# Optimization experiments

Measured on AMD Instinct MI355X. Metric: run time of the kernel, lower is better.

Reference implementation:

```python
import jax, jax.numpy as jnp
import numpy as np

B, S, D = 2, 2048, 1024
FFN = 4096
E, TOPK = 4, 2
H, WIN = 8, 128
EPS = 1e-6


def rmsnorm(x, w):
    rms = jax.lax.rsqrt(jnp.mean(x * x, axis=-1, keepdims=True) + EPS)
    return x * rms * w


def linear_scan(x, a):
    """h_t = a_t * h_{t-1} + x_t along axis=1, via associative scan."""
    def comb(c1, c2):
        a1, x1 = c1
        a2, x2 = c2
        return (a1 * a2, a2 * x1 + x2)
    _, h = jax.lax.associative_scan(comb, (a, x), axis=1)
    return h


def mingru_expert(xn, Wg, bg, Wv, bv, Wd, bd):
    g = xn @ Wg + bg
    v = xn @ Wv + bv
    d = xn @ Wd + bd
    x_scan = jax.nn.sigmoid(g) * jnp.tanh(v)
    a = 0.001 + 0.998 * jax.nn.sigmoid(d)
    return linear_scan(x_scan, a)


def setup_inputs() -> dict:
    key = jax.random.key(0)
    ks = jax.random.split(key, 16)
    sc = 0.02
    return {
        "x": jax.random.normal(ks[0], (B, S, D), jnp.float32),
        "rms_mix_w": jnp.ones((D,), jnp.float32),
        "gate_w": jax.random.normal(ks[1], (D, E), jnp.float32) * sc,
        "Wg": jax.random.normal(ks[2], (E, D, D), jnp.float32) * sc,
        "bg": jnp.zeros((E, D), jnp.float32),
        "Wv": jax.random.normal(ks[3], (E, D, D), jnp.float32) * sc,
        "bv": jnp.zeros((E, D), jnp.float32),
        "Wd": jax.random.normal(ks[4], (E, D, D), jnp.float32) * sc,
        "bd": jnp.ones((E, D), jnp.float32),  # decay_bias_init = 1.0
        "rms_attn_w": jnp.ones((D,), jnp.float32),
        "w_qkv": jax.random.normal(ks[5], (D, 3 * D), jnp.float32) * sc,
        "w_attn_out": jax.random.normal(ks[6], (D, D), jnp.float32) * sc,
        "rms_ffn_w": jnp.ones((D,), jnp.float32),
        "w_ffn_gate": jax.random.normal(ks[7], (D, FFN), jnp.float32) * sc,
        "w_ffn_up": jax.random.normal(ks[8], (D, FFN), jnp.float32) * sc,
        "w_ffn_out": jax.random.normal(ks[9], (FFN, D), jnp.float32) * sc,
    }


def reference(x, rms_mix_w, gate_w, Wg, bg, Wv, bv, Wd, bd,
              rms_attn_w, w_qkv, w_attn_out,
              rms_ffn_w, w_ffn_gate, w_ffn_up, w_ffn_out):
    # --- MoE-MinGRU mixer -------------------------------------------------
    xn = rmsnorm(x, rms_mix_w)
    gate_logits = xn @ gate_w                         # [B,S,E]
    top_vals, top_idx = jax.lax.top_k(gate_logits, TOPK)
    weights = jax.nn.softmax(top_vals, axis=-1)       # [B,S,K]
    expert_outs = jax.vmap(mingru_expert, in_axes=(None, 0, 0, 0, 0, 0, 0))(
        xn, Wg, bg, Wv, bv, Wd, bd)                   # [E,B,S,D]
    expert_outs = jnp.moveaxis(expert_outs, 0, 2)     # [B,S,E,D]
    gathered = jnp.take_along_axis(expert_outs, top_idx[..., None], axis=2)  # [B,S,K,D]
    mix = jnp.sum(weights[..., None] * gathered, axis=2)
    x = x + mix

    # --- Sliding-window causal attention ----------------------------------
    xn = rmsnorm(x, rms_attn_w)
    dh = D // H
    qkv = (xn @ w_qkv).reshape(B, S, 3, H, dh)
    q, k, v = qkv[:, :, 0], qkv[:, :, 1], qkv[:, :, 2]  # [B,S,H,dh]
    scores = jnp.einsum("bqhd,bkhd->bhqk", q, k) / jnp.sqrt(jnp.float32(dh))
    i = jnp.arange(S)[:, None]
    j = jnp.arange(S)[None, :]
    allowed = (j <= i) & (j > i - WIN)
    scores = jnp.where(allowed, scores, -jnp.inf)
    attn = jax.nn.softmax(scores, axis=-1)
    ao = jnp.einsum("bhqk,bkhd->bqhd", attn, v).reshape(B, S, D)
    x = x + ao @ w_attn_out

    # --- SwiGLU FFN --------------------------------------------------------
    xn = rmsnorm(x, rms_ffn_w)
    ffn = (jax.nn.silu(xn @ w_ffn_gate) * (xn @ w_ffn_up)) @ w_ffn_out
    return x + ffn
```

## Files before the change

kernel.cpp:

```cpp
#include <hip/hip_runtime.h>
#include <hip/hip_bf16.h>
#include <math.h>

constexpr int kB   = 2;
constexpr int kS   = 2048;
constexpr int kD   = 1024;
constexpr int kFFN = 4096;
constexpr int kM   = kB * kS;
constexpr int kH   = 8;
constexpr int kDH  = 128;
constexpr int kNC  = 64;
constexpr int kT   = kS / kNC;
constexpr int kNE  = 12288;

typedef unsigned short u16;
typedef __attribute__((ext_vector_type(8))) short short8;
typedef __attribute__((ext_vector_type(4))) float f32x4;

__device__ __forceinline__ float sigf(float x) { return 1.0f / (1.0f + __expf(-x)); }
__device__ __forceinline__ float bu2f(u16 u) { return __uint_as_float(((unsigned)u) << 16); }
__device__ __forceinline__ u16 f2bu(float f) {
    __hip_bfloat16 h = __float2bfloat16(f);
    return reinterpret_cast<u16&>(h);
}
__device__ __forceinline__ void async16(const void* g, void* l) {
    __builtin_amdgcn_global_load_lds((const __attribute__((address_space(1))) void*)g,
                                     (__attribute__((address_space(3))) void*)l, 16, 0, 0);
}

__global__ __launch_bounds__(256) void rmsnorm_k(const float* __restrict__ x,
                                                 const float* __restrict__ w,
                                                 u16* __restrict__ o)
{
    __shared__ float red[4];
    const int row = blockIdx.x;
    const int t = threadIdx.x;
    float4 v = ((const float4*)(x + (size_t)row * kD))[t];
    float ss = v.x*v.x + v.y*v.y + v.z*v.z + v.w*v.w;
    #pragma unroll
    for (int m = 32; m; m >>= 1) ss += __shfl_xor(ss, m);
    if ((t & 63) == 0) red[t >> 6] = ss;
    __syncthreads();
    float tot = red[0] + red[1] + red[2] + red[3];
    float r = rsqrtf(tot * (1.0f / (float)kD) + 1e-6f);
    float4 wv = ((const float4*)w)[t];
    ushort4 u;
    u.x = f2bu(v.x * r * wv.x); u.y = f2bu(v.y * r * wv.y);
    u.z = f2bu(v.z * r * wv.z); u.w = f2bu(v.w * r * wv.w);
    ((ushort4*)(o + (size_t)row * kD))[t] = u;
}

__global__ __launch_bounds__(64) void routing_k(const float* __restrict__ x,
                                                const float* __restrict__ wmix,
                                                const float* __restrict__ gw,
                                                float* __restrict__ wts,
                                                int* __restrict__ idx)
{
    const int row = blockIdx.x;
    const int lane = threadIdx.x;
    const float* xr = x + (size_t)row * kD;
    float ss = 0.0f;
    for (int d = lane; d < kD; d += 64) { float v = xr[d]; ss = fmaf(v, v, ss); }
    #pragma unroll
    for (int m = 32; m; m >>= 1) ss += __shfl_xor(ss, m);
    float r = rsqrtf(ss * (1.0f / (float)kD) + 1e-6f);

    float a0 = 0, a1 = 0, a2 = 0, a3 = 0;
    for (int d = lane; d < kD; d += 64) {
        float xv = xr[d] * wmix[d];
        float4 g = ((const float4*)gw)[d];
        a0 = fmaf(xv, g.x, a0);
        a1 = fmaf(xv, g.y, a1);
        a2 = fmaf(xv, g.z, a2);
        a3 = fmaf(xv, g.w, a3);
    }
    #pragma unroll
    for (int m = 32; m; m >>= 1) {
        a0 += __shfl_xor(a0, m);
        a1 += __shfl_xor(a1, m);
        a2 += __shfl_xor(a2, m);
        a3 += __shfl_xor(a3, m);
    }
    if (lane == 0) {
        float a[4] = {a0, a1, a2, a3};
        int i0 = 0; float v0 = a[0];
        #pragma unroll
        for (int e = 1; e < 4; ++e) if (a[e] > v0) { v0 = a[e]; i0 = e; }
        int i1 = -1; float v1 = -INFINITY;
        #pragma unroll
        for (int e = 0; e < 4; ++e) if (e != i0 && a[e] > v1) { v1 = a[e]; i1 = e; }
        float e1 = __expf(r * (v1 - v0));
        float dn = 1.0f + e1;
        wts[row * 2 + 0] = 1.0f / dn;
        wts[row * 2 + 1] = e1 / dn;
        idx[row * 2 + 0] = i0;
        idx[row * 2 + 1] = i1;
    }
}

__global__ __launch_bounds__(256) void transp_k(const float* __restrict__ src,
                                                u16* __restrict__ dst,
                                                int rows, int cols,
                                                size_t sstride, size_t dstride)
{
    __shared__ float t[32][33];
    const float* s = src + blockIdx.z * sstride;
    u16* d = dst + blockIdx.z * dstride;
    const int c0 = blockIdx.x * 32, r0 = blockIdx.y * 32;
    const int tc = threadIdx.x & 31, tr4 = (threadIdx.x >> 5) * 4;
    #pragma unroll
    for (int i = 0; i < 4; ++i)
        t[tr4 + i][tc] = s[(size_t)(r0 + tr4 + i) * cols + c0 + tc];
    __syncthreads();
    #pragma unroll
    for (int i = 0; i < 4; ++i) {
        int cc = tr4 + i;
        d[(size_t)(c0 + cc) * rows + r0 + tc] = f2bu(t[tc][cc]);
    }
}

__global__ __launch_bounds__(256) void biaspack_k(const float* __restrict__ bg,
                                                  const float* __restrict__ bv,
                                                  const float* __restrict__ bd,
                                                  float* __restrict__ pb)
{
    int e = blockIdx.y;
    int r = blockIdx.x * 256 + threadIdx.x;
    const float* src = (r < 1024) ? bg : (r < 2048) ? bv : bd;
    pb[e * 3072 + r] = src[e * 1024 + (r & 1023)];
}

template<bool BIAS, bool SILU, bool MUL>
__global__ __launch_bounds__(512, 2) void gemm256_k(
    const u16* __restrict__ A, const u16* __restrict__ BT,
    const float* __restrict__ bias, const u16* __restrict__ mulsrc,
    u16* __restrict__ Cout, int N, int K)
{
    __shared__ __align__(16) u16 lds[3 * 24576];
    const int tid = threadIdx.x;
    const int l = tid & 63;
    const int w = tid >> 6;
    const int wr = w >> 1, wc = w & 1;
    const int fr = l & 15, g = l >> 4;

    const int gx = gridDim.x;
    const int nwg = gx * gridDim.y;
    const int orig = blockIdx.y * gx + blockIdx.x;
    const int xcd = orig & 7;
    const int q8 = nwg >> 3, r8 = nwg & 7;
    const int wg = (xcd < r8 ? xcd * (q8 + 1) : r8 * (q8 + 1) + (xcd - r8) * q8) + (orig >> 3);
    const int bm = (wg / gx) * 256, bn = (wg % gx) * 128;

    const int srow = l >> 3;
    const int scol = (l & 7) ^ srow;
    const u16* gA = A  + (size_t)(bm + srow) * K + scol * 8;
    const u16* gB = BT + (size_t)(bn + srow) * K + scol * 8;

    auto STAGE = [&](int kt, int sb) {
        u16* dst = lds + sb * 24576 + l * 8;
        const int k0 = kt * 64;
        #pragma unroll
        for (int i = 0; i < 4; ++i) {
            int chunk = w * 4 + i;
            async16(gA + (size_t)chunk * 8 * K + k0, dst + chunk * 512);
        }
        #pragma unroll
        for (int i = 0; i < 2; ++i) {
            int chunk = w * 2 + i;
            async16(gB + (size_t)chunk * 8 * K + k0, dst + 16384 + chunk * 512);
        }
    };

    f32x4 acc[4][4];
    #pragma unroll
    for (int m = 0; m < 4; ++m)
        #pragma unroll
        for (int n = 0; n < 4; ++n) acc[m][n] = (f32x4){0.f, 0.f, 0.f, 0.f};

    STAGE(0, 0);
    STAGE(1, 1);
    const int nt = K >> 6;
    int cs = 0;
    for (int t = 0; t < nt; ++t) {
        if (t + 1 < nt) asm volatile("s_waitcnt vmcnt(6)" ::: "memory");
        else            asm volatile("s_waitcnt vmcnt(0)" ::: "memory");
        __builtin_amdgcn_s_barrier();
        __builtin_amdgcn_sched_barrier(0);
        if (t + 2 < nt) {
            int ns = cs + 2; if (ns >= 3) ns -= 3;
            STAGE(t + 2, ns);
        }
        const u16* bA = lds + cs * 24576;
        const u16* bB = bA + 16384;
        #pragma unroll
        for (int ks = 0; ks < 2; ++ks) {
            short8 a[4], b[4];
            const int xo = ((ks * 4 + g) ^ (fr & 7)) * 8;
            #pragma unroll
            for (int m = 0; m < 4; ++m)
                a[m] = *(const short8*)(bA + (wr * 64 + m * 16 + fr) * 64 + xo);
            #pragma unroll
            for (int n = 0; n < 4; ++n)
                b[n] = *(const short8*)(bB + (wc * 64 + n * 16 + fr) * 64 + xo);
            #pragma unroll
            for (int m = 0; m < 4; ++m)
                #pragma unroll
                for (int n = 0; n < 4; ++n)
                    acc[m][n] = __builtin_amdgcn_mfma_f32_16x16x32_bf16(a[m], b[n], acc[m][n], 0, 0, 0);
        }
        cs = (cs == 2) ? 0 : cs + 1;
    }

    const int orow0 = bm + wr * 64 + g * 4;
    const int ocol0 = bn + wc * 64 + fr;
    float bi[4];
    if constexpr (BIAS) {
        #pragma unroll
        for (int n = 0; n < 4; ++n) bi[n] = bias[ocol0 + n * 16];
    }
    #pragma unroll
    for (int m = 0; m < 4; ++m) {
        #pragma unroll
        for (int r = 0; r < 4; ++r) {
            const size_t ro = (size_t)(orow0 + m * 16 + r) * N;
            #pragma unroll
            for (int n = 0; n < 4; ++n) {
                const size_t off = ro + ocol0 + n * 16;
                float v = acc[m][n][r];
                if constexpr (BIAS) v += bi[n];
                if constexpr (SILU) v = v * sigf(v);
                if constexpr (MUL)  v *= bu2f(mulsrc[off]);
                Cout[off] = f2bu(v);
            }
        }
    }
}

template<int WN, bool BIAS, bool RES, bool SILU, bool MUL, bool OBF>
__global__ __launch_bounds__(256, 2) void gemm_bf16_k(
    const u16* __restrict__ A, const u16* __restrict__ BT,
    const float* __restrict__ bias, const float* __restrict__ res,
    const u16* __restrict__ mulsrc, void* __restrict__ Cout,
    int N, int K)
{
    constexpr int BN = 32 * WN;
    __shared__ __align__(16) u16 As[2][128 * 32];
    __shared__ __align__(16) u16 Bs[2][BN * 32];
    const int tid = threadIdx.x;
    const int lane = tid & 63;
    const int w = tid >> 6;
    const int wr = w >> 1, wc = w & 1;

    const int gx = gridDim.x;
    const int nwg = gx * gridDim.y;
    const int orig = blockIdx.y * gx + blockIdx.x;
    const int xcd = orig & 7;
    const int q8 = nwg >> 3, r8 = nwg & 7;
    const int wg = (xcd < r8 ? xcd * (q8 + 1) : r8 * (q8 + 1) + (xcd - r8) * q8) + (orig >> 3);
    const int bm = (wg / gx) * 128, bn = (wg % gx) * BN;

    const int fr = lane & 15, fk = (lane >> 4) * 8;

    const u16* gA1 = A + (size_t)(bm + (tid >> 2)) * K + (tid & 3) * 8;
    const u16* gA2 = gA1 + (size_t)64 * K;
    const u16* gB1 = BT + (size_t)(bn + (tid >> 2)) * K + (tid & 3) * 8;
    const u16* gB2 = gB1 + (size_t)64 * K;

    f32x4 acc[4][WN];
    #pragma unroll
    for (int m = 0; m < 4; ++m)
        #pragma unroll
        for (int n = 0; n < WN; ++n) acc[m][n] = (f32x4){0.f, 0.f, 0.f, 0.f};

    const int paOff = (wr * 64 + fr) * 32 + fk;
    const int pbOff = (wc * WN * 16 + fr) * 32 + fk;

    async16(gA1, As[0] + tid * 8);
    async16(gA2, As[0] + (256 + tid) * 8);
    async16(gB1, Bs[0] + tid * 8);
    if constexpr (WN == 4) async16(gB2, Bs[0] + (256 + tid) * 8);
    __syncthreads();

    int cur = 0;
    for (int k0 = 0; k0 < K; k0 += 32) {
        if (k0 + 32 < K) {
            const int nb = cur ^ 1;
            async16(gA1 + k0 + 32, As[nb] + tid * 8);
            async16(gA2 + k0 + 32, As[nb] + (256 + tid) * 8);
            async16(gB1 + k0 + 32, Bs[nb] + tid * 8);
            if constexpr (WN == 4) async16(gB2 + k0 + 32, Bs[nb] + (256 + tid) * 8);
        }
        const u16* pa = As[cur] + paOff;
        const u16* pb = Bs[cur] + pbOff;
        short8 a[4], b[WN];
        #pragma unroll
        for (int m = 0; m < 4; ++m) a[m] = *(const short8*)(pa + m * 512);
        #pragma unroll
        for (int n = 0; n < WN; ++n) b[n] = *(const short8*)(pb + n * 512);
        #pragma unroll
        for (int m = 0; m < 4; ++m)
            #pragma unroll
            for (int n = 0; n < WN; ++n)
                acc[m][n] = __builtin_amdgcn_mfma_f32_16x16x32_bf16(a[m], b[n], acc[m][n], 0, 0, 0);
        __syncthreads();
        cur ^= 1;
    }

    const int orow0 = bm + wr * 64 + ((lane >> 4) << 2);
    const int ocol0 = bn + wc * WN * 16 + fr;
    float bi[WN];
    if constexpr (BIAS) {
        #pragma unroll
        for (int n = 0; n < WN; ++n) bi[n] = bias[ocol0 + n * 16];
    }
    #pragma unroll
    for (int m = 0; m < 4; ++m) {
        #pragma unroll
        for (int r = 0; r < 4; ++r) {
            const int row = orow0 + m * 16 + r;
            const size_t ro = (size_t)row * N;
            #pragma unroll
            for (int n = 0; n < WN; ++n) {
                const size_t off = ro + ocol0 + n * 16;
                float v = acc[m][n][r];
                if constexpr (BIAS) v += bi[n];
                if constexpr (SILU) v = v * sigf(v);
                if constexpr (MUL)  v *= bu2f(mulsrc[off]);
                if constexpr (RES)  v += res[off];
                if constexpr (OBF)  ((u16*)Cout)[off] = f2bu(v);
                else                ((float*)Cout)[off] = v;
            }
        }
    }
}

__global__ __launch_bounds__(256) void scan1_k(const u16* __restrict__ gvdall,
                                               float* __restrict__ sumA,
                                               float* __restrict__ sumX)
{
    const int e = blockIdx.y;
    int i = blockIdx.x * 256 + threadIdx.x;
    int d = i & (kD - 1);
    int c = (i >> 10) & (kNC - 1);
    int b = i >> 16;
    const u16* gvd = gvdall + e * 3072;
    size_t base = ((size_t)b * kS + c * kT) * kNE + d;
    float A = 1.0f, X = 0.0f;
    for (int t = 0; t < kT; ++t) {
        size_t ix = base + (size_t)t * kNE;
        float xs = sigf(bu2f(gvd[ix])) * tanhf(bu2f(gvd[ix + 1024]));
        float a  = 0.001f + 0.998f * sigf(bu2f(gvd[ix + 2048]));
        A *= a;
        X = fmaf(a, X, xs);
    }
    size_t si = ((size_t)(e * kNC + c) * kB + b) * kD + d;
    sumA[si] = A;
    sumX[si] = X;
}

__global__ __launch_bounds__(256) void scan2_k(const float* __restrict__ sumA,
                                               const float* __restrict__ sumX,
                                               float* __restrict__ carry)
{
    const int e = blockIdx.y;
    int bd = blockIdx.x * 256 + threadIdx.x;
    float h = 0.0f;
    for (int c = 0; c < kNC; ++c) {
        size_t si = ((size_t)(e * kNC + c)) * (kB * kD) + bd;
        carry[si] = h;
        h = fmaf(sumA[si], h, sumX[si]);
    }
}

__global__ __launch_bounds__(256) void scan3_k(const u16* __restrict__ gvdall,
                                               const float* __restrict__ carry,
                                               u16* __restrict__ ehb)
{
    const int e = blockIdx.y;
    int i = blockIdx.x * 256 + threadIdx.x;
    int d = i & (kD - 1);
    int c = (i >> 10) & (kNC - 1);
    int b = i >> 16;
    const u16* gvd = gvdall + e * 3072;
    size_t base = ((size_t)b * kS + c * kT) * kNE + d;
    size_t obase = (size_t)e * kM * kD + ((size_t)b * kS + c * kT) * kD + d;
    float h = carry[((size_t)(e * kNC + c) * kB + b) * kD + d];
    for (int t = 0; t < kT; ++t) {
        size_t ix = base + (size_t)t * kNE;
        float xs = sigf(bu2f(gvd[ix])) * tanhf(bu2f(gvd[ix + 1024]));
        float a  = 0.001f + 0.998f * sigf(bu2f(gvd[ix + 2048]));
        h = fmaf(a, h, xs);
        ehb[obase + (size_t)t * kD] = f2bu(h);
    }
}

__global__ __launch_bounds__(256) void mix_k(const float* __restrict__ x,
                                             const u16* __restrict__ ehb,
                                             const float* __restrict__ wts,
                                             const int* __restrict__ idx,
                                             float* __restrict__ xo)
{
    size_t i = (size_t)blockIdx.x * 256 + threadIdx.x;
    int m = (int)(i >> 8);
    float w0 = wts[m * 2 + 0], w1 = wts[m * 2 + 1];
    int e0 = idx[m * 2 + 0], e1 = idx[m * 2 + 1];
    size_t MD4 = (size_t)kM * (kD / 4);
    float4 xv = ((const float4*)x)[i];
    ushort4 h0 = ((const ushort4*)ehb)[(size_t)e0 * MD4 + i];
    ushort4 h1 = ((const ushort4*)ehb)[(size_t)e1 * MD4 + i];
    float4 o;
    o.x = xv.x + w0 * bu2f(h0.x) + w1 * bu2f(h1.x);
    o.y = xv.y + w0 * bu2f(h0.y) + w1 * bu2f(h1.y);
    o.z = xv.z + w0 * bu2f(h0.z) + w1 * bu2f(h1.z);
    o.w = xv.w + w0 * bu2f(h0.w) + w1 * bu2f(h1.w);
    ((float4*)xo)[i] = o;
}

__global__ __launch_bounds__(256) void transpV_k(const u16* __restrict__ qkvb,
                                                 u16* __restrict__ vT)
{
    __shared__ u16 t[64][68];
    const int tid = threadIdx.x;
    const int s0 = blockIdx.x * 64;
    const int d0 = blockIdx.y * 64;
    const int bh = blockIdx.z;
    const int bb = bh >> 3, hh = bh & 7;
    const u16* src = qkvb + (size_t)(bb * kS + s0) * 3072 + 2048 + hh * kDH + d0;
    for (int idx = tid; idx < 64 * 16; idx += 256) {
        int sl = idx >> 4, c4 = (idx & 15) * 4;
        *(ushort4*)&t[sl][c4] = *(const ushort4*)(src + (size_t)sl * 3072 + c4);
    }
    __syncthreads();
    u16* dst = vT + ((size_t)bh * kDH + d0) * kS + s0;
    for (int idx = tid; idx < 64 * 16; idx += 256) {
        int dl = idx >> 4, s4 = (idx & 15) * 4;
        ushort4 v;
        v.x = t[s4 + 0][dl]; v.y = t[s4 + 1][dl];
        v.z = t[s4 + 2][dl]; v.w = t[s4 + 3][dl];
        *(ushort4*)(dst + (size_t)dl * kS + s4) = v;
    }
}

__global__ __launch_bounds__(256) void attn_mfma_k(const u16* __restrict__ qkvb,
                                                   const u16* __restrict__ vT,
                                                   u16* __restrict__ aob)
{
    __shared__ __align__(16) u16 KV[26112];
    __shared__ __align__(16) u16 P[4 * 16 * 200];

    const int tid = threadIdx.x;
    const int lane = tid & 63;
    const int w = tid >> 6;
    const int fr = lane & 15, g = lane >> 4;
    const int q0 = blockIdx.x * 64;
    const int hh = blockIdx.y;
    const int bb = blockIdx.z;
    const int kbase = q0 - 128;
    const float scale = 0.08838834764831845f;

    const u16* qkv_b = qkvb + (size_t)bb * kS * 3072 + hh * kDH;

    for (int idx = tid; idx < 192 * 16; idx += 256) {
        int k = idx >> 4, c = idx & 15;
        int kg = kbase + k; if (kg < 0) kg = 0;
        short8 v = *(const short8*)(qkv_b + (size_t)kg * 3072 + 1024 + c * 8);
        *(short8*)(&KV[k * 136 + c * 8]) = v;
    }
    short8 qf[4];
    {
        const u16* qrow = qkv_b + (size_t)(q0 + w * 16 + fr) * 3072 + g * 8;
        #pragma unroll
        for (int s = 0; s < 4; ++s) qf[s] = *(const short8*)(qrow + s * 32);
    }
    __syncthreads();

    f32x4 sacc[12];
    #pragma unroll
    for (int f = 0; f < 12; ++f) sacc[f] = (f32x4){0.f, 0.f, 0.f, 0.f};
    #pragma unroll
    for (int s = 0; s < 4; ++s) {
        #pragma unroll
        for (int f = 0; f < 12; ++f) {
            short8 bfr = *(const short8*)(&KV[(f * 16 + fr) * 136 + s * 32 + g * 8]);
            sacc[f] = __builtin_amdgcn_mfma_f32_16x16x32_bf16(qf[s], bfr, sacc[f], 0, 0, 0);
        }
    }

    float p[12][4];
    #pragma unroll
    for (int r = 0; r < 4; ++r) {
        const int ql = w * 16 + g * 4 + r;
        int kmin = 128 - q0; if (kmin < ql + 1) kmin = ql + 1;
        const int kmax = ql + 128;
        float mx = -1e30f;
        #pragma unroll
        for (int f = 0; f < 12; ++f) {
            int kl = f * 16 + fr;
            float sv = (kl >= kmin && kl <= kmax) ? sacc[f][r] * scale : -1e30f;
            p[f][r] = sv;
            mx = fmaxf(mx, sv);
        }
        mx = fmaxf(mx, __shfl_xor(mx, 1));
        mx = fmaxf(mx, __shfl_xor(mx, 2));
        mx = fmaxf(mx, __shfl_xor(mx, 4));
        mx = fmaxf(mx, __shfl_xor(mx, 8));
        float l = 0.f;
        #pragma unroll
        for (int f = 0; f < 12; ++f) { float e = __expf(p[f][r] - mx); p[f][r] = e; l += e; }
        l += __shfl_xor(l, 1);
        l += __shfl_xor(l, 2);
        l += __shfl_xor(l, 4);
        l += __shfl_xor(l, 8);
        float linv = 1.0f / l;
        #pragma unroll
        for (int f = 0; f < 12; ++f) p[f][r] *= linv;
    }

    {
        u16* pw = &P[(w * 16) * 200];
        #pragma unroll
        for (int r = 0; r < 4; ++r)
            #pragma unroll
            for (int f = 0; f < 12; ++f)
                pw[(g * 4 + r) * 200 + f * 16 + fr] = f2bu(p[f][r]);
    }
    __syncthreads();

    {
        const u16* vrow = vT + (size_t)(bb * kH + hh) * kDH * kS;
        for (int idx = tid; idx < 128 * 25; idx += 256) {
            int d = idx / 25, c = idx % 25;
            if (c < 24) {
                int s0k = kbase + c * 8;
                short8 v;
                if (s0k < 0) v = (short8){0, 0, 0, 0, 0, 0, 0, 0};
                else v = *(const short8*)(vrow + (size_t)d * kS + s0k);
                *(short8*)(&KV[d * 200 + c * 8]) = v;
            }
        }
    }
    __syncthreads();

    f32x4 oacc[8];
    #pragma unroll
    for (int f = 0; f < 8; ++f) oacc[f] = (f32x4){0.f, 0.f, 0.f, 0.f};
    const u16* pr = &P[(w * 16 + fr) * 200 + g * 8];
    #pragma unroll
    for (int s = 0; s < 6; ++s) {
        short8 afr = *(const short8*)(pr + s * 32);
        #pragma unroll
        for (int f = 0; f < 8; ++f) {
            short8 bfr = *(const short8*)(&KV[(f * 16 + fr) * 200 + s * 32 + g * 8]);
            oacc[f] = __builtin_amdgcn_mfma_f32_16x16x32_bf16(afr, bfr, oacc[f], 0, 0, 0);
        }
    }
    u16* orow = aob + ((size_t)(bb * kS + q0 + w * 16 + g * 4) * kD) + hh * kDH + fr;
    #pragma unroll
    for (int r = 0; r < 4; ++r)
        #pragma unroll
        for (int f = 0; f < 8; ++f)
            orow[(size_t)r * kD + f * 16] = f2bu(oacc[f][r]);
}

extern "C" void kernel_launch(void* const* d_in, const int* in_sizes, int n_in,
                              void* d_out, int out_size, void* d_ws, size_t ws_size,
                              hipStream_t stream)
{
    (void)in_sizes; (void)n_in; (void)out_size; (void)ws_size;

    const float* x          = (const float*)d_in[0];
    const float* rms_mix    = (const float*)d_in[1];
    const float* gate_w     = (const float*)d_in[2];
    const float* Wg         = (const float*)d_in[3];
    const float* bg         = (const float*)d_in[4];
    const float* Wv         = (const float*)d_in[5];
    const float* bv         = (const float*)d_in[6];
    const float* Wd         = (const float*)d_in[7];
    const float* bd         = (const float*)d_in[8];
    const float* rms_attn   = (const float*)d_in[9];
    const float* w_qkv      = (const float*)d_in[10];
    const float* w_attn_out = (const float*)d_in[11];
    const float* rms_ffn    = (const float*)d_in[12];
    const float* w_ffn_gate = (const float*)d_in[13];
    const float* w_ffn_up   = (const float*)d_in[14];
    const float* w_ffn_out  = (const float*)d_in[15];
    float* out = (float*)d_out;

    const size_t MD = (size_t)kM * kD;
    const size_t M1 = 1024ull * 1024;
    char* p = (char*)d_ws;
    auto take = [&](size_t n) { char* r = p; p += (n + 255) & ~(size_t)255; return r; };

    u16*   xnb    = (u16*)take(MD * 2);
    u16*   gvdall = (u16*)take((size_t)kM * kNE * 2);
    u16*   qkvb   = gvdall;
    u16*   hidA   = gvdall;
    u16*   hidB   = gvdall + (size_t)kM * kFFN;
    u16*   ehb    = (u16*)take(4 * MD * 2);
    u16*   aob    = ehb;
    u16*   vTb    = ehb + MD;
    u16*   wbuf   = (u16*)take(12ull * M1 * 2);
    float* pbias  = (float*)take((size_t)kNE * 4);
    float* sumA   = (float*)take(4ull * kNC * kB * kD * 4);
    float* sumX   = (float*)take(4ull * kNC * kB * kD * 4);
    float* carry  = (float*)take(4ull * kNC * kB * kD * 4);
    float* wts    = (float*)take((size_t)2 * kM * 4);
    int*   tidx   = (int*)take((size_t)2 * kM * 4);

    const dim3 blk(256);

    transp_k<<<dim3(32, 32, 4), blk, 0, stream>>>(Wg, wbuf, 1024, 1024,
                                                  (size_t)kD * kD, 3 * M1);
    transp_k<<<dim3(32, 32, 4), blk, 0, stream>>>(Wv, wbuf + M1, 1024, 1024,
                                                  (size_t)kD * kD, 3 * M1);
    transp_k<<<dim3(32, 32, 4), blk, 0, stream>>>(Wd, wbuf + 2 * M1, 1024, 1024,
                                                  (size_t)kD * kD, 3 * M1);
    biaspack_k<<<dim3(12, 4), blk, 0, stream>>>(bg, bv, bd, pbias);

    rmsnorm_k<<<kM, blk, 0, stream>>>(x, rms_mix, xnb);
    routing_k<<<kM, dim3(64), 0, stream>>>(x, rms_mix, gate_w, wts, tidx);

    gemm256_k<true, false, false><<<dim3(kNE / 128, kM / 256), dim3(512), 0, stream>>>(
        xnb, wbuf, pbias, nullptr, gvdall, kNE, 1024);
    const int scan_blocks = kB * kD * kNC / 256;
    scan1_k<<<dim3(scan_blocks, 4), blk, 0, stream>>>(gvdall, sumA, sumX);
    scan2_k<<<dim3(kB * kD / 256, 4), blk, 0, stream>>>(sumA, sumX, carry);
    scan3_k<<<dim3(scan_blocks, 4), blk, 0, stream>>>(gvdall, carry, ehb);

    mix_k<<<(int)(MD / 1024), blk, 0, stream>>>(x, ehb, wts, tidx, out);

    rmsnorm_k<<<kM, blk, 0, stream>>>(out, rms_attn, xnb);
    transp_k<<<dim3(96, 32, 1), blk, 0, stream>>>(w_qkv, wbuf, 1024, 3072, 0, 0);
    gemm256_k<false, false, false><<<dim3(3072 / 128, kM / 256), dim3(512), 0, stream>>>(
        xnb, wbuf, nullptr, nullptr, qkvb, 3072, 1024);
    transpV_k<<<dim3(kS / 64, 2, kB * kH), blk, 0, stream>>>(qkvb, vTb);
    attn_mfma_k<<<dim3(kS / 64, kH, kB), blk, 0, stream>>>(qkvb, vTb, aob);
    transp_k<<<dim3(32, 32, 1), blk, 0, stream>>>(w_attn_out, wbuf + 3 * M1, 1024, 1024, 0, 0);
    gemm_bf16_k<2, false, true, false, false, false><<<dim3(1024 / 64, kM / 128), blk, 0, stream>>>(
        aob, wbuf + 3 * M1, nullptr, out, nullptr, out, 1024, 1024);

    rmsnorm_k<<<kM, blk, 0, stream>>>(out, rms_ffn, xnb);
    transp_k<<<dim3(128, 32, 1), blk, 0, stream>>>(w_ffn_gate, wbuf + 4 * M1, 1024, 4096, 0, 0);
    transp_k<<<dim3(128, 32, 1), blk, 0, stream>>>(w_ffn_up, wbuf + 8 * M1, 1024, 4096, 0, 0);
    transp_k<<<dim3(32, 128, 1), blk, 0, stream>>>(w_ffn_out, wbuf, 4096, 1024, 0, 0);
    gemm256_k<false, true, false><<<dim3(kFFN / 128, kM / 256), dim3(512), 0, stream>>>(
        xnb, wbuf + 4 * M1, nullptr, nullptr, hidA, kFFN, 1024);
    gemm256_k<false, false, true><<<dim3(kFFN / 128, kM / 256), dim3(512), 0, stream>>>(
        xnb, wbuf + 8 * M1, nullptr, hidA, hidB, kFFN, 1024);
    gemm_bf16_k<2, false, true, false, false, false><<<dim3(1024 / 64, kM / 128), blk, 0, stream>>>(
        hidB, wbuf, nullptr, out, nullptr, out, 1024, 4096);
}
```

Measured before the change: 528.3 us.

## Interleave GEMM prefetch with MFMA sub-steps and write scan output only to routed slots

The 256x128 GEMM main loop now issues the next-stage async loads in two halves, one per k-substep, after the LDS fragment reads. It adds an lgkmcnt wait, raises wave priority around the MFMA block, and inserts an extra barrier between substeps, so global loads overlap with compute more evenly. Separately, the scan kernel now writes each expert's hidden state only into the routed top-k slot buffers instead of all four expert outputs. This cuts write traffic to two dense buffers that the mix kernel reads without indexing. The trade-off is a per-token index lookup and branch inside the scan loop, plus an extra barrier per GEMM iteration.

```diff
diff --git a/kernel.cpp b/kernel.cpp
--- a/kernel.cpp
+++ b/kernel.cpp
@@ -156,19 +156,14 @@
     const u16* gA = A  + (size_t)(bm + srow) * K + scol * 8;
     const u16* gB = BT + (size_t)(bn + srow) * K + scol * 8;
 
-    auto STAGE = [&](int kt, int sb) {
+    auto STAGE_P = [&](int kt, int sb, int part) {
         u16* dst = lds + sb * 24576 + l * 8;
         const int k0 = kt * 64;
-        #pragma unroll
-        for (int i = 0; i < 4; ++i) {
-            int chunk = w * 4 + i;
-            async16(gA + (size_t)chunk * 8 * K + k0, dst + chunk * 512);
-        }
-        #pragma unroll
-        for (int i = 0; i < 2; ++i) {
-            int chunk = w * 2 + i;
-            async16(gB + (size_t)chunk * 8 * K + k0, dst + 16384 + chunk * 512);
-        }
+        const int a0 = w * 4 + part * 2;
+        async16(gA + (size_t)(a0 + 0) * 8 * K + k0, dst + (a0 + 0) * 512);
+        async16(gA + (size_t)(a0 + 1) * 8 * K + k0, dst + (a0 + 1) * 512);
+        const int b0 = w * 2 + part;
+        async16(gB + (size_t)b0 * 8 * K + k0, dst + 16384 + b0 * 512);
     };
 
     f32x4 acc[4][4];
@@ -177,8 +172,8 @@
         #pragma unroll
         for (int n = 0; n < 4; ++n) acc[m][n] = (f32x4){0.f, 0.f, 0.f, 0.f};
 
-    STAGE(0, 0);
-    STAGE(1, 1);
+    STAGE_P(0, 0, 0); STAGE_P(0, 0, 1);
+    STAGE_P(1, 1, 0); STAGE_P(1, 1, 1);
     const int nt = K >> 6;
     int cs = 0;
     for (int t = 0; t < nt; ++t) {
@@ -186,12 +181,9 @@
         else            asm volatile("s_waitcnt vmcnt(0)" ::: "memory");
         __builtin_amdgcn_s_barrier();
         __builtin_amdgcn_sched_barrier(0);
-        if (t + 2 < nt) {
-            int ns = cs + 2; if (ns >= 3) ns -= 3;
-            STAGE(t + 2, ns);
-        }
         const u16* bA = lds + cs * 24576;
         const u16* bB = bA + 16384;
+        int ns = cs + 2; if (ns >= 3) ns -= 3;
         #pragma unroll
         for (int ks = 0; ks < 2; ++ks) {
             short8 a[4], b[4];
@@ -202,11 +194,19 @@
             #pragma unroll
             for (int n = 0; n < 4; ++n)
                 b[n] = *(const short8*)(bB + (wc * 64 + n * 16 + fr) * 64 + xo);
+            if (t + 2 < nt) STAGE_P(t + 2, ns, ks);
+            __builtin_amdgcn_sched_barrier(0);
+            asm volatile("s_waitcnt lgkmcnt(0)" ::: "memory");
+            __builtin_amdgcn_sched_barrier(0);
+            __builtin_amdgcn_s_setprio(1);
             #pragma unroll
             for (int m = 0; m < 4; ++m)
                 #pragma unroll
                 for (int n = 0; n < 4; ++n)
                     acc[m][n] = __builtin_amdgcn_mfma_f32_16x16x32_bf16(a[m], b[n], acc[m][n], 0, 0, 0);
+            __builtin_amdgcn_s_setprio(0);
+            __builtin_amdgcn_sched_barrier(0);
+            if (ks == 0) __builtin_amdgcn_s_barrier();
         }
         cs = (cs == 2) ? 0 : cs + 1;
     }
@@ -374,7 +374,9 @@
 
 __global__ __launch_bounds__(256) void scan3_k(const u16* __restrict__ gvdall,
                                                const float* __restrict__ carry,
-                                               u16* __restrict__ ehb)
+                                               const int* __restrict__ tidx,
+                                               u16* __restrict__ slot0,
+                                               u16* __restrict__ slot1)
 {
     const int e = blockIdx.y;
     int i = blockIdx.x * 256 + threadIdx.x;
@@ -383,31 +385,32 @@
     int b = i >> 16;
     const u16* gvd = gvdall + e * 3072;
     size_t base = ((size_t)b * kS + c * kT) * kNE + d;
-    size_t obase = (size_t)e * kM * kD + ((size_t)b * kS + c * kT) * kD + d;
     float h = carry[((size_t)(e * kNC + c) * kB + b) * kD + d];
+    const int tok0 = b * kS + c * kT;
     for (int t = 0; t < kT; ++t) {
         size_t ix = base + (size_t)t * kNE;
         float xs = sigf(bu2f(gvd[ix])) * tanhf(bu2f(gvd[ix + 1024]));
         float a  = 0.001f + 0.998f * sigf(bu2f(gvd[ix + 2048]));
         h = fmaf(a, h, xs);
-        ehb[obase + (size_t)t * kD] = f2bu(h);
+        const int tok = tok0 + t;
+        const size_t o = (size_t)tok * kD + d;
+        if (e == tidx[tok * 2])          slot0[o] = f2bu(h);
+        else if (e == tidx[tok * 2 + 1]) slot1[o] = f2bu(h);
     }
 }
 
 __global__ __launch_bounds__(256) void mix_k(const float* __restrict__ x,
-                                             const u16* __restrict__ ehb,
+                                             const u16* __restrict__ slot0,
+                                             const u16* __restrict__ slot1,
                                              const float* __restrict__ wts,
-                                             const int* __restrict__ idx,
                                              float* __restrict__ xo)
 {
     size_t i = (size_t)blockIdx.x * 256 + threadIdx.x;
     int m = (int)(i >> 8);
     float w0 = wts[m * 2 + 0], w1 = wts[m * 2 + 1];
-    int e0 = idx[m * 2 + 0], e1 = idx[m * 2 + 1];
-    size_t MD4 = (size_t)kM * (kD / 4);
     float4 xv = ((const float4*)x)[i];
-    ushort4 h0 = ((const ushort4*)ehb)[(size_t)e0 * MD4 + i];
-    ushort4 h1 = ((const ushort4*)ehb)[(size_t)e1 * MD4 + i];
+    ushort4 h0 = ((const ushort4*)slot0)[i];
+    ushort4 h1 = ((const ushort4*)slot1)[i];
     float4 o;
     o.x = xv.x + w0 * bu2f(h0.x) + w1 * bu2f(h1.x);
     o.y = xv.y + w0 * bu2f(h0.y) + w1 * bu2f(h1.y);
@@ -597,6 +600,8 @@
     u16*   hidA   = gvdall;
     u16*   hidB   = gvdall + (size_t)kM * kFFN;
     u16*   ehb    = (u16*)take(4 * MD * 2);
+    u16*   slot0  = ehb;
+    u16*   slot1  = ehb + MD;
     u16*   aob    = ehb;
     u16*   vTb    = ehb + MD;
     u16*   wbuf   = (u16*)take(12ull * M1 * 2);
@@ -625,9 +630,9 @@
     const int scan_blocks = kB * kD * kNC / 256;
     scan1_k<<<dim3(scan_blocks, 4), blk, 0, stream>>>(gvdall, sumA, sumX);
     scan2_k<<<dim3(kB * kD / 256, 4), blk, 0, stream>>>(sumA, sumX, carry);
-    scan3_k<<<dim3(scan_blocks, 4), blk, 0, stream>>>(gvdall, carry, ehb);
-
-    mix_k<<<(int)(MD / 1024), blk, 0, stream>>>(x, ehb, wts, tidx, out);
+    scan3_k<<<dim3(scan_blocks, 4), blk, 0, stream>>>(gvdall, carry, tidx, slot0, slot1);
+
+    mix_k<<<(int)(MD / 1024), blk, 0, stream>>>(x, slot0, slot1, wts, out);
 
     rmsnorm_k<<<kM, blk, 0, stream>>>(out, rms_attn, xnb);
     transp_k<<<dim3(96, 32, 1), blk, 0, stream>>>(w_qkv, wbuf, 1024, 3072, 0, 0);
```

Result: no change. 535.4 us (+1.4%).

## Use 256x256 tiles for main GEMMs, new output GEMM, write only routed experts

Applied to the files above, without the earlier changes.

The main bf16 GEMM moves from 256x128 to 256x256 tiles with double buffering and per-iteration syncthreads, replacing the earlier three-stage vmcnt pipeline. The output-projection GEMMs get a new 256x64 kernel with a three-stage async pipeline that fuses the residual add. The scan now writes only the hidden states of each token's two selected experts into two slot buffers, so the mix kernel no longer gathers from all four expert outputs. The trade-offs are fewer blocks for the large GEMMs (occupancy and tail risk), higher register pressure from 128 accumulators, and loss of the deeper pipeline in gemmA.

```diff
diff --git a/kernel.cpp b/kernel.cpp
--- a/kernel.cpp
+++ b/kernel.cpp
@@ -27,6 +27,11 @@
     __builtin_amdgcn_global_load_lds((const __attribute__((address_space(1))) void*)g,
                                      (__attribute__((address_space(3))) void*)l, 16, 0, 0);
 }
+__device__ __forceinline__ int xcd_swz(int orig, int nwg) {
+    const int xcd = orig & 7;
+    const int q8 = nwg >> 3, r8 = nwg & 7;
+    return (xcd < r8 ? xcd * (q8 + 1) : r8 * (q8 + 1) + (xcd - r8) * q8) + (orig >> 3);
+}
 
 __global__ __launch_bounds__(256) void rmsnorm_k(const float* __restrict__ x,
                                                  const float* __restrict__ w,
@@ -131,25 +136,21 @@
 }
 
 template<bool BIAS, bool SILU, bool MUL>
-__global__ __launch_bounds__(512, 2) void gemm256_k(
+__global__ __launch_bounds__(512, 2) void gemmA_k(
     const u16* __restrict__ A, const u16* __restrict__ BT,
     const float* __restrict__ bias, const u16* __restrict__ mulsrc,
     u16* __restrict__ Cout, int N, int K)
 {
-    __shared__ __align__(16) u16 lds[3 * 24576];
+    __shared__ __align__(16) u16 lds[2][32768];
     const int tid = threadIdx.x;
     const int l = tid & 63;
     const int w = tid >> 6;
-    const int wr = w >> 1, wc = w & 1;
+    const int wr = w >> 2, wc = w & 3;
     const int fr = l & 15, g = l >> 4;
 
     const int gx = gridDim.x;
-    const int nwg = gx * gridDim.y;
-    const int orig = blockIdx.y * gx + blockIdx.x;
-    const int xcd = orig & 7;
-    const int q8 = nwg >> 3, r8 = nwg & 7;
-    const int wg = (xcd < r8 ? xcd * (q8 + 1) : r8 * (q8 + 1) + (xcd - r8) * q8) + (orig >> 3);
-    const int bm = (wg / gx) * 256, bn = (wg % gx) * 128;
+    const int wg = xcd_swz(blockIdx.y * gx + blockIdx.x, gx * gridDim.y);
+    const int bm = (wg / gx) * 256, bn = (wg % gx) * 256;
 
     const int srow = l >> 3;
     const int scol = (l & 7) ^ srow;
@@ -157,61 +158,49 @@
     const u16* gB = BT + (size_t)(bn + srow) * K + scol * 8;
 
     auto STAGE = [&](int kt, int sb) {
-        u16* dst = lds + sb * 24576 + l * 8;
+        u16* dst = lds[sb] + l * 8;
         const int k0 = kt * 64;
         #pragma unroll
         for (int i = 0; i < 4; ++i) {
             int chunk = w * 4 + i;
             async16(gA + (size_t)chunk * 8 * K + k0, dst + chunk * 512);
-        }
-        #pragma unroll
-        for (int i = 0; i < 2; ++i) {
-            int chunk = w * 2 + i;
             async16(gB + (size_t)chunk * 8 * K + k0, dst + 16384 + chunk * 512);
         }
     };
 
-    f32x4 acc[4][4];
-    #pragma unroll
-    for (int m = 0; m < 4; ++m)
+    f32x4 acc[8][4];
+    #pragma unroll
+    for (int m = 0; m < 8; ++m)
         #pragma unroll
         for (int n = 0; n < 4; ++n) acc[m][n] = (f32x4){0.f, 0.f, 0.f, 0.f};
 
     STAGE(0, 0);
-    STAGE(1, 1);
+    __syncthreads();
     const int nt = K >> 6;
-    int cs = 0;
     for (int t = 0; t < nt; ++t) {
-        if (t + 1 < nt) asm volatile("s_waitcnt vmcnt(6)" ::: "memory");
-        else            asm volatile("s_waitcnt vmcnt(0)" ::: "memory");
-        __builtin_amdgcn_s_barrier();
-        __builtin_amdgcn_sched_barrier(0);
-        if (t + 2 < nt) {
-            int ns = cs + 2; if (ns >= 3) ns -= 3;
-            STAGE(t + 2, ns);
-        }
-        const u16* bA = lds + cs * 24576;
-        const u16* bB = bA + 16384;
+        const int cb = t & 1;
+        if (t + 1 < nt) STAGE(t + 1, cb ^ 1);
+        const u16* bA = lds[cb];
+        const u16* bB = lds[cb] + 16384;
         #pragma unroll
         for (int ks = 0; ks < 2; ++ks) {
-            short8 a[4], b[4];
             const int xo = ((ks * 4 + g) ^ (fr & 7)) * 8;
-            #pragma unroll
-            for (int m = 0; m < 4; ++m)
-                a[m] = *(const short8*)(bA + (wr * 64 + m * 16 + fr) * 64 + xo);
+            short8 b[4];
             #pragma unroll
             for (int n = 0; n < 4; ++n)
                 b[n] = *(const short8*)(bB + (wc * 64 + n * 16 + fr) * 64 + xo);
             #pragma unroll
-            for (int m = 0; m < 4; ++m)
+            for (int m = 0; m < 8; ++m) {
+                short8 a = *(const short8*)(bA + (wr * 128 + m * 16 + fr) * 64 + xo);
                 #pragma unroll
                 for (int n = 0; n < 4; ++n)
-                    acc[m][n] = __builtin_amdgcn_mfma_f32_16x16x32_bf16(a[m], b[n], acc[m][n], 0, 0, 0);
-        }
-        cs = (cs == 2) ? 0 : cs + 1;
-    }
-
-    const int orow0 = bm + wr * 64 + g * 4;
+                    acc[m][n] = __builtin_amdgcn_mfma_f32_16x16x32_bf16(a, b[n], acc[m][n], 0, 0, 0);
+            }
+        }
+        __syncthreads();
+    }
+
+    const int orow0 = bm + wr * 128 + g * 4;
     const int ocol0 = bn + wc * 64 + fr;
     float bi[4];
     if constexpr (BIAS) {
@@ -219,7 +208,7 @@
         for (int n = 0; n < 4; ++n) bi[n] = bias[ocol0 + n * 16];
     }
     #pragma unroll
-    for (int m = 0; m < 4; ++m) {
+    for (int m = 0; m < 8; ++m) {
         #pragma unroll
         for (int r = 0; r < 4; ++r) {
             const size_t ro = (size_t)(orow0 + m * 16 + r) * N;
@@ -236,99 +225,92 @@
     }
 }
 
-template<int WN, bool BIAS, bool RES, bool SILU, bool MUL, bool OBF>
-__global__ __launch_bounds__(256, 2) void gemm_bf16_k(
+__global__ __launch_bounds__(256, 2) void gemmO_k(
     const u16* __restrict__ A, const u16* __restrict__ BT,
-    const float* __restrict__ bias, const float* __restrict__ res,
-    const u16* __restrict__ mulsrc, void* __restrict__ Cout,
+    const float* __restrict__ res, float* __restrict__ Cout,
     int N, int K)
 {
-    constexpr int BN = 32 * WN;
-    __shared__ __align__(16) u16 As[2][128 * 32];
-    __shared__ __align__(16) u16 Bs[2][BN * 32];
+    __shared__ __align__(16) u16 lds[3][20480];
     const int tid = threadIdx.x;
-    const int lane = tid & 63;
+    const int l = tid & 63;
     const int w = tid >> 6;
-    const int wr = w >> 1, wc = w & 1;
+    const int fr = l & 15, g = l >> 4;
 
     const int gx = gridDim.x;
-    const int nwg = gx * gridDim.y;
-    const int orig = blockIdx.y * gx + blockIdx.x;
-    const int xcd = orig & 7;
-    const int q8 = nwg >> 3, r8 = nwg & 7;
-    const int wg = (xcd < r8 ? xcd * (q8 + 1) : r8 * (q8 + 1) + (xcd - r8) * q8) + (orig >> 3);
-    const int bm = (wg / gx) * 128, bn = (wg % gx) * BN;
-
-    const int fr = lane & 15, fk = (lane >> 4) * 8;
-
-    const u16* gA1 = A + (size_t)(bm + (tid >> 2)) * K + (tid & 3) * 8;
-    const u16* gA2 = gA1 + (size_t)64 * K;
-    const u16* gB1 = BT + (size_t)(bn + (tid >> 2)) * K + (tid & 3) * 8;
-    const u16* gB2 = gB1 + (size_t)64 * K;
-
-    f32x4 acc[4][WN];
+    const int wg = xcd_swz(blockIdx.y * gx + blockIdx.x, gx * gridDim.y);
+    const int bm = (wg / gx) * 256, bn = (wg % gx) * 64;
+
+    const int srow = l >> 3;
+    const int scol = (l & 7) ^ srow;
+    const u16* gA = A  + (size_t)(bm + srow) * K + scol * 8;
+    const u16* gB = BT + (size_t)(bn + srow) * K + scol * 8;
+
+    auto STAGE = [&](int kt, int sb) {
+        u16* dst = lds[sb] + l * 8;
+        const int k0 = kt * 64;
+        #pragma unroll
+        for (int i = 0; i < 8; ++i) {
+            int chunk = w * 8 + i;
+            async16(gA + (size_t)chunk * 8 * K + k0, dst + chunk * 512);
+        }
+        #pragma unroll
+        for (int i = 0; i < 2; ++i) {
+            int chunk = w * 2 + i;
+            async16(gB + (size_t)chunk * 8 * K + k0, dst + 16384 + chunk * 512);
+        }
+    };
+
+    f32x4 acc[4][4];
     #pragma unroll
     for (int m = 0; m < 4; ++m)
         #pragma unroll
-        for (int n = 0; n < WN; ++n) acc[m][n] = (f32x4){0.f, 0.f, 0.f, 0.f};
-
-    const int paOff = (wr * 64 + fr) * 32 + fk;
-    const int pbOff = (wc * WN * 16 + fr) * 32 + fk;
-
-    async16(gA1, As[0] + tid * 8);
-    async16(gA2, As[0] + (256 + tid) * 8);
-    async16(gB1, Bs[0] + tid * 8);
-    if constexpr (WN == 4) async16(gB2, Bs[0] + (256 + tid) * 8);
-    __syncthreads();
-
-    int cur = 0;
-    for (int k0 = 0; k0 < K; k0 += 32) {
-        if (k0 + 32 < K) {
-            const int nb = cur ^ 1;
-            async16(gA1 + k0 + 32, As[nb] + tid * 8);
-            async16(gA2 + k0 + 32, As[nb] + (256 + tid) * 8);
-            async16(gB1 + k0 + 32, Bs[nb] + tid * 8);
-            if constexpr (WN == 4) async16(gB2 + k0 + 32, Bs[nb] + (256 + tid) * 8);
-        }
-        const u16* pa = As[cur] + paOff;
-        const u16* pb = Bs[cur] + pbOff;
-        short8 a[4], b[WN];
-        #pragma unroll
-        for (int m = 0; m < 4; ++m) a[m] = *(const short8*)(pa + m * 512);
-        #pragma unroll
-        for (int n = 0; n < WN; ++n) b[n] = *(const short8*)(pb + n * 512);
-        #pragma unroll
-        for (int m = 0; m < 4; ++m)
-            #pragma unroll
-            for (int n = 0; n < WN; ++n)
-                acc[m][n] = __builtin_amdgcn_mfma_f32_16x16x32_bf16(a[m], b[n], acc[m][n], 0, 0, 0);
-        __syncthreads();
-        cur ^= 1;
-    }
-
-    const int orow0 = bm + wr * 64 + ((lane >> 4) << 2);
-    const int ocol0 = bn + wc * WN * 16 + fr;
-    float bi[WN];
-    if constexpr (BIAS) {
-        #pragma unroll
-        for (int n = 0; n < WN; ++n) bi[n] = bias[ocol0 + n * 16];
-    }
+        for (int n = 0; n < 4; ++n) acc[m][n] = (f32x4){0.f, 0.f, 0.f, 0.f};
+
+    STAGE(0, 0);
+    STAGE(1, 1);
+    const int nt = K >> 6;
+    int cs = 0;
+    for (int t = 0; t < nt; ++t) {
+        if (t + 1 < nt) asm volatile("s_waitcnt vmcnt(10)" ::: "memory");
+        else            asm volatile("s_waitcnt vmcnt(0)" ::: "memory");
+        __builtin_amdgcn_s_barrier();
+        __builtin_amdgcn_sched_barrier(0);
+        if (t + 2 < nt) {
+            int ns = cs + 2; if (ns >= 3) ns -= 3;
+            STAGE(t + 2, ns);
+        }
+        const u16* bA = lds[cs];
+        const u16* bB = lds[cs] + 16384;
+        #pragma unroll
+        for (int ks = 0; ks < 2; ++ks) {
+            const int xo = ((ks * 4 + g) ^ (fr & 7)) * 8;
+            short8 a[4], b[4];
+            #pragma unroll
+            for (int m = 0; m < 4; ++m)
+                a[m] = *(const short8*)(bA + (w * 64 + m * 16 + fr) * 64 + xo);
+            #pragma unroll
+            for (int n = 0; n < 4; ++n)
+                b[n] = *(const short8*)(bB + (n * 16 + fr) * 64 + xo);
+            #pragma unroll
+            for (int m = 0; m < 4; ++m)
+                #pragma unroll
+                for (int n = 0; n < 4; ++n)
+                    acc[m][n] = __builtin_amdgcn_mfma_f32_16x16x32_bf16(a[m], b[n], acc[m][n], 0, 0, 0);
+        }
+        cs = (cs == 2) ? 0 : cs + 1;
+    }
+
+    const int orow0 = bm + w * 64 + g * 4;
+    const int ocol0 = bn + fr;
     #pragma unroll
     for (int m = 0; m < 4; ++m) {
         #pragma unroll
         for (int r = 0; r < 4; ++r) {
-            const int row = orow0 + m * 16 + r;
-            const size_t ro = (size_t)row * N;
-            #pragma unroll
-            for (int n = 0; n < WN; ++n) {
+            const size_t ro = (size_t)(orow0 + m * 16 + r) * N;
+            #pragma unroll
+            for (int n = 0; n < 4; ++n) {
                 const size_t off = ro + ocol0 + n * 16;
-                float v = acc[m][n][r];
-                if constexpr (BIAS) v += bi[n];
-                if constexpr (SILU) v = v * sigf(v);
-                if constexpr (MUL)  v *= bu2f(mulsrc[off]);
-                if constexpr (RES)  v += res[off];
-                if constexpr (OBF)  ((u16*)Cout)[off] = f2bu(v);
-                else                ((float*)Cout)[off] = v;
+                Cout[off] = acc[m][n][r] + res[off];
             }
         }
     }
@@ -374,7 +356,9 @@
 
 __global__ __launch_bounds__(256) void scan3_k(const u16* __restrict__ gvdall,
                                                const float* __restrict__ carry,
-                                               u16* __restrict__ ehb)
+                                               const int* __restrict__ tidx,
+                                               u16* __restrict__ slot0,
+                                               u16* __restrict__ slot1)
 {
     const int e = blockIdx.y;
     int i = blockIdx.x * 256 + threadIdx.x;
@@ -383,31 +367,32 @@
     int b = i >> 16;
     const u16* gvd = gvdall + e * 3072;
     size_t base = ((size_t)b * kS + c * kT) * kNE + d;
-    size_t obase = (size_t)e * kM * kD + ((size_t)b * kS + c * kT) * kD + d;
     float h = carry[((size_t)(e * kNC + c) * kB + b) * kD + d];
+    const int tok0 = b * kS + c * kT;
     for (int t = 0; t < kT; ++t) {
         size_t ix = base + (size_t)t * kNE;
         float xs = sigf(bu2f(gvd[ix])) * tanhf(bu2f(gvd[ix + 1024]));
         float a  = 0.001f + 0.998f * sigf(bu2f(gvd[ix + 2048]));
         h = fmaf(a, h, xs);
-        ehb[obase + (size_t)t * kD] = f2bu(h);
+        const int tok = tok0 + t;
+        const size_t o = (size_t)tok * kD + d;
+        if (e == tidx[tok * 2])          slot0[o] = f2bu(h);
+        else if (e == tidx[tok * 2 + 1]) slot1[o] = f2bu(h);
     }
 }
 
 __global__ __launch_bounds__(256) void mix_k(const float* __restrict__ x,
-                                             const u16* __restrict__ ehb,
+                                             const u16* __restrict__ slot0,
+                                             const u16* __restrict__ slot1,
                                              const float* __restrict__ wts,
-                                             const int* __restrict__ idx,
                                              float* __restrict__ xo)
 {
     size_t i = (size_t)blockIdx.x * 256 + threadIdx.x;
     int m = (int)(i >> 8);
     float w0 = wts[m * 2 + 0], w1 = wts[m * 2 + 1];
-    int e0 = idx[m * 2 + 0], e1 = idx[m * 2 + 1];
-    size_t MD4 = (size_t)kM * (kD / 4);
     float4 xv = ((const float4*)x)[i];
-    ushort4 h0 = ((const ushort4*)ehb)[(size_t)e0 * MD4 + i];
-    ushort4 h1 = ((const ushort4*)ehb)[(size_t)e1 * MD4 + i];
+    ushort4 h0 = ((const ushort4*)slot0)[i];
+    ushort4 h1 = ((const ushort4*)slot1)[i];
     float4 o;
     o.x = xv.x + w0 * bu2f(h0.x) + w1 * bu2f(h1.x);
     o.y = xv.y + w0 * bu2f(h0.y) + w1 * bu2f(h1.y);
@@ -597,6 +582,8 @@
     u16*   hidA   = gvdall;
     u16*   hidB   = gvdall + (size_t)kM * kFFN;
     u16*   ehb    = (u16*)take(4 * MD * 2);
+    u16*   slot0  = ehb;
+    u16*   slot1  = ehb + MD;
     u16*   aob    = ehb;
     u16*   vTb    = ehb + MD;
     u16*   wbuf   = (u16*)take(12ull * M1 * 2);
@@ -620,33 +607,33 @@
     rmsnorm_k<<<kM, blk, 0, stream>>>(x, rms_mix, xnb);
     routing_k<<<kM, dim3(64), 0, stream>>>(x, rms_mix, gate_w, wts, tidx);
 
-    gemm256_k<true, false, false><<<dim3(kNE / 128, kM / 256), dim3(512), 0, stream>>>(
+    gemmA_k<true, false, false><<<dim3(kNE / 256, kM / 256), dim3(512), 0, stream>>>(
         xnb, wbuf, pbias, nullptr, gvdall, kNE, 1024);
     const int scan_blocks = kB * kD * kNC / 256;
     scan1_k<<<dim3(scan_blocks, 4), blk, 0, stream>>>(gvdall, sumA, sumX);
     scan2_k<<<dim3(kB * kD / 256, 4), blk, 0, stream>>>(sumA, sumX, carry);
-    scan3_k<<<dim3(scan_blocks, 4), blk, 0, stream>>>(gvdall, carry, ehb);
-
-    mix_k<<<(int)(MD / 1024), blk, 0, stream>>>(x, ehb, wts, tidx, out);
+    scan3_k<<<dim3(scan_blocks, 4), blk, 0, stream>>>(gvdall, carry, tidx, slot0, slot1);
+
+    mix_k<<<(int)(MD / 1024), blk, 0, stream>>>(x, slot0, slot1, wts, out);
 
     rmsnorm_k<<<kM, blk, 0, stream>>>(out, rms_attn, xnb);
     transp_k<<<dim3(96, 32, 1), blk, 0, stream>>>(w_qkv, wbuf, 1024, 3072, 0, 0);
-    gemm256_k<false, false, false><<<dim3(3072 / 128, kM / 256), dim3(512), 0, stream>>>(
+    gemmA_k<false, false, false><<<dim3(3072 / 256, kM / 256), dim3(512), 0, stream>>>(
         xnb, wbuf, nullptr, nullptr, qkvb, 3072, 1024);
     transpV_k<<<dim3(kS / 64, 2, kB * kH), blk, 0, stream>>>(qkvb, vTb);
     attn_mfma_k<<<dim3(kS / 64, kH, kB), blk, 0, stream>>>(qkvb, vTb, aob);
     transp_k<<<dim3(32, 32, 1), blk, 0, stream>>>(w_attn_out, wbuf + 3 * M1, 1024, 1024, 0, 0);
-    gemm_bf16_k<2, false, true, false, false, false><<<dim3(1024 / 64, kM / 128), blk, 0, stream>>>(
-        aob, wbuf + 3 * M1, nullptr, out, nullptr, out, 1024, 1024);
+    gemmO_k<<<dim3(1024 / 64, kM / 256), blk, 0, stream>>>(
+        aob, wbuf + 3 * M1, out, out, 1024, 1024);
 
     rmsnorm_k<<<kM, blk, 0, stream>>>(out, rms_ffn, xnb);
     transp_k<<<dim3(128, 32, 1), blk, 0, stream>>>(w_ffn_gate, wbuf + 4 * M1, 1024, 4096, 0, 0);
     transp_k<<<dim3(128, 32, 1), blk, 0, stream>>>(w_ffn_up, wbuf + 8 * M1, 1024, 4096, 0, 0);
     transp_k<<<dim3(32, 128, 1), blk, 0, stream>>>(w_ffn_out, wbuf, 4096, 1024, 0, 0);
-    gemm256_k<false, true, false><<<dim3(kFFN / 128, kM / 256), dim3(512), 0, stream>>>(
+    gemmA_k<false, true, false><<<dim3(kFFN / 256, kM / 256), dim3(512), 0, stream>>>(
         xnb, wbuf + 4 * M1, nullptr, nullptr, hidA, kFFN, 1024);
-    gemm256_k<false, false, true><<<dim3(kFFN / 128, kM / 256), dim3(512), 0, stream>>>(
+    gemmA_k<false, false, true><<<dim3(kFFN / 256, kM / 256), dim3(512), 0, stream>>>(
         xnb, wbuf + 8 * M1, nullptr, hidA, hidB, kFFN, 1024);
-    gemm_bf16_k<2, false, true, false, false, false><<<dim3(1024 / 64, kM / 128), blk, 0, stream>>>(
-        hidB, wbuf, nullptr, out, nullptr, out, 1024, 4096);
-}
+    gemmO_k<<<dim3(1024 / 64, kM / 256), blk, 0, stream>>>(
+        hidB, wbuf, out, out, 1024, 4096);
+}
```

Measured after the change: 479.1 us. 9.3% less time.
